# Kernel tuning notes

Hardware: AMD Instinct MI355X
Metric: run time of the kernel (lower is better)

Reference implementation:

```python
import jax, jax.numpy as jnp
import numpy as np

N, E = 50000, 800000
IN_C, HID, OUT_C = 128, 128, 64
EPS = 1e-5


def layer_norm(x, gamma, beta):
    mu = jnp.mean(x, axis=-1, keepdims=True)
    var = jnp.mean(jnp.square(x - mu), axis=-1, keepdims=True)
    return (x - mu) * jax.lax.rsqrt(var + EPS) * gamma + beta


def sage_conv(h, src, dst, W_l, b_l, W_r):
    # PyG SAGEConv (aggr='mean'): out = lin_l(mean_{j in N(i)} h_j) + lin_r(h_i)
    msg = h[src]                                                   # [E, HID] gather
    s = jax.ops.segment_sum(msg, dst, num_segments=N)              # [N, HID]
    cnt = jax.ops.segment_sum(jnp.ones((src.shape[0], 1), h.dtype), dst, num_segments=N)
    mean = s / jnp.maximum(cnt, 1.0)
    return mean @ W_l + b_l + h @ W_r


def setup_inputs() -> dict:
    key = jax.random.key(0)
    ks = jax.random.split(key, 12)
    sd_in = 1.0 / np.sqrt(IN_C)
    sd_h = 1.0 / np.sqrt(HID)
    return {
        "x": jax.random.normal(ks[0], (N, IN_C), jnp.float32),
        "edge_index": jax.random.randint(ks[1], (2, E), 0, N, jnp.int32),
        "edge_attr": jax.random.normal(ks[2], (E, IN_C), jnp.float32),
        "W_ne": jax.random.uniform(ks[3], (IN_C, HID), jnp.float32, -sd_in, sd_in),
        "b_ne": jax.random.uniform(ks[4], (HID,), jnp.float32, -sd_in, sd_in),
        "W_l": jax.random.uniform(ks[5], (HID, HID), jnp.float32, -sd_h, sd_h),
        "b_l": jax.random.uniform(ks[6], (HID,), jnp.float32, -sd_h, sd_h),
        "W_r": jax.random.uniform(ks[7], (HID, HID), jnp.float32, -sd_h, sd_h),
        "gamma": jnp.ones((HID,), jnp.float32),
        "beta": jnp.zeros((HID,), jnp.float32),
        "W_lin": jax.random.uniform(ks[8], (HID, OUT_C), jnp.float32, -sd_h, sd_h),
        "b_lin": jax.random.uniform(ks[9], (OUT_C,), jnp.float32, -sd_h, sd_h),
    }


def reference(x, edge_index, edge_attr, W_ne, b_ne, W_l, b_l, W_r, gamma, beta, W_lin, b_lin):
    src, dst = edge_index[0], edge_index[1]
    # node encoder
    h = x @ W_ne + b_ne
    # pre-conv with layers[0].conv
    h = sage_conv(h, src, dst, W_l, b_l, W_r)
    # layers[0] is unfixed: LN -> ReLU -> dropout(eval=id) -> conv -> residual
    r = layer_norm(h, gamma, beta)
    r = jax.nn.relu(r)
    h = sage_conv(r, src, dst, W_l, b_l, W_r) + h
    # layers[1:] are fixed -> identity
    # final norm/act/dropout(eval=id)/lin (reuses layers[0].norm/act)
    o = jax.nn.relu(layer_norm(h, gamma, beta))
    return o @ W_lin + b_lin
```

## Files before the change

### kernel.cpp

```cpp
#include <hip/hip_runtime.h>

typedef __attribute__((ext_vector_type(8))) short bf16x8;
typedef __attribute__((ext_vector_type(4))) float f32x4;

constexpr float LN_EPS = 1e-5f;

__device__ inline ushort f2bf(float f) {
  uint u = __float_as_uint(f);
  u += 0x7FFF + ((u >> 16) & 1);
  return (ushort)(u >> 16);
}
__device__ inline float bflo(uint u) { return __uint_as_float(u << 16); }
__device__ inline float bfhi(uint u) { return __uint_as_float(u & 0xFFFF0000u); }
__device__ inline uint pk2(float lo, float hi) { return (uint)f2bf(lo) | ((uint)f2bf(hi) << 16); }

struct Params {
  const float* x; const int* ei;
  const float *W_ne, *b_ne, *W_l, *b_l, *W_r, *gamma, *beta, *W_lin, *b_lin;
  float* out;
  ushort *Qbf, *H1, *Dbf, *xbf, *WAt, *WBt, *Wlt, *Wrt, *Wlint;
  signed char* Aq;
  float* Ascale;
  float *bA, *bB;
  int *cnt, *incl, *rowptr, *cursor, *bsums, *srclist;
  int N, E, nbS, nbT;
};


__global__ __launch_bounds__(256) void k_hist(Params p) {
  int e = blockIdx.x * 256 + threadIdx.x;
  if (e < p.E) atomicAdd(&p.cnt[p.ei[p.E + e]], 1);
}

__global__ __launch_bounds__(256) void k_p2(Params p) {
  __shared__ int sh[256];
  const int tid = threadIdx.x, bid = blockIdx.x;
  if (bid < p.nbS) {
    int i = bid * 256 + tid;
    int v = (i < p.N) ? p.cnt[i] : 0;
    sh[tid] = v;
    __syncthreads();
    for (int off = 1; off < 256; off <<= 1) {
      int t = (tid >= off) ? sh[tid - off] : 0;
      __syncthreads();
      sh[tid] += t;
      __syncthreads();
    }
    if (i < p.N) p.incl[i] = sh[tid];
    if (tid == 255) p.bsums[bid] = sh[255];
  } else if (bid < p.nbS + 129) {
    int blk = bid - p.nbS;
    float* srow = (float*)sh;
    const float* src = (blk < 128) ? (p.W_ne + blk * 128) : p.b_ne;
    if (tid < 128) srow[tid] = src[tid];
    __syncthreads();
    int col = tid & 127;
    const float* Wx = (tid < 128) ? p.W_l : p.W_r;
    float acc = 0.f;
#pragma unroll 8
    for (int k = 0; k < 128; ++k) acc = fmaf(srow[k], Wx[k * 128 + col], acc);
    if (blk < 128) {
      ushort* dst = (tid < 128) ? p.WAt : p.WBt;
      dst[col * 128 + blk] = f2bf(acc);
    } else {
      float* dst = (tid < 128) ? p.bA : p.bB;
      dst[col] = acc;
    }
  } else {
    const int nx16 = p.N * 16;
    const int total = nx16 + 16384 + 16384 + 8192;
    const int i0 = (bid - (p.nbS + 129)) * 256 + tid;
    const int st = (gridDim.x - (p.nbS + 129)) * 256;
    const float4* xin = (const float4*)p.x;
    uint4* xo = (uint4*)p.xbf;
    for (int idx = i0; idx < total; idx += st) {
      if (idx < nx16) {
        float4 a = xin[2 * (size_t)idx], b = xin[2 * (size_t)idx + 1];
        uint4 v;
        v.x = pk2(a.x, a.y); v.y = pk2(a.z, a.w);
        v.z = pk2(b.x, b.y); v.w = pk2(b.z, b.w);
        xo[idx] = v;
        continue;
      }
      int t = idx - nx16;
      if (t < 16384) { p.Wlt[(t & 127) * 128 + (t >> 7)] = f2bf(p.W_l[t]); continue; }
      t -= 16384;
      if (t < 16384) { p.Wrt[(t & 127) * 128 + (t >> 7)] = f2bf(p.W_r[t]); continue; }
      t -= 16384;
      p.Wlint[(t & 63) * 128 + (t >> 6)] = f2bf(p.W_lin[t]);
    }
  }
}

__global__ __launch_bounds__(256) void k_fill(Params p) {
  int e = blockIdx.x * 256 + threadIdx.x;
  if (e >= p.E) return;
  int s = p.ei[e], d = p.ei[p.E + e];
  int pos = atomicAdd(&p.cursor[d], 1);
  p.srclist[pos] = s;
}


template <int NCOL, int OMODE>
__device__ __forceinline__ void gemm_tile(const ushort* __restrict__ X, const ushort* __restrict__ Wt,
                                          const float* __restrict__ bias, void* __restrict__ Yv,
                                          float* __restrict__ Yscale, int M, int tile, char* ldsraw) {
  constexpr int NF = NCOL / 32;
  const int tid = threadIdx.x;
  const int wave = tid >> 6, lane = tid & 63;
  const int rbase = (wave >> 1) * 64;
  const int cbase = (wave & 1) * (NCOL / 2);
  const int lrow = lane & 15;
  const int lkb = (lane >> 4) * 8;
  const int row0 = tile * 128;

  size_t rIdx[4];
#pragma unroll
  for (int mf = 0; mf < 4; ++mf) {
    int r = row0 + rbase + mf * 16 + lrow;
    rIdx[mf] = (size_t)((r < M) ? r : (M - 1));
  }

  f32x4 acc[4][NF];
#pragma unroll
  for (int mf = 0; mf < 4; ++mf)
#pragma unroll
    for (int nf = 0; nf < NF; ++nf) acc[mf][nf] = (f32x4){0.f, 0.f, 0.f, 0.f};

#pragma unroll
  for (int ks = 0; ks < 4; ++ks) {
    bf16x8 a[4], b[NF];
#pragma unroll
    for (int mf = 0; mf < 4; ++mf)
      a[mf] = *(const bf16x8*)(X + rIdx[mf] * 128 + ks * 32 + lkb);
#pragma unroll
    for (int nf = 0; nf < NF; ++nf)
      b[nf] = *(const bf16x8*)(Wt + (size_t)(cbase + nf * 16 + lrow) * 128 + ks * 32 + lkb);
#pragma unroll
    for (int mf = 0; mf < 4; ++mf)
#pragma unroll
      for (int nf = 0; nf < NF; ++nf)
        acc[mf][nf] = __builtin_amdgcn_mfma_f32_16x16x32_bf16(a[mf], b[nf], acc[mf][nf], 0, 0, 0);
  }

  if (bias) {
#pragma unroll
    for (int nf = 0; nf < NF; ++nf) {
      float bv = bias[cbase + nf * 16 + lrow];
#pragma unroll
      for (int mf = 0; mf < 4; ++mf)
#pragma unroll
        for (int r = 0; r < 4; ++r) acc[mf][nf][r] += bv;
    }
  }

  if constexpr (OMODE == 2) {
    float (*rmaxh)[2] = (float(*)[2])ldsraw;
    signed char (*qt)[128] = (signed char(*)[128])(ldsraw + 1024);
#pragma unroll
    for (int mf = 0; mf < 4; ++mf)
#pragma unroll
      for (int r = 0; r < 4; ++r) {
        float m = 0.f;
#pragma unroll
        for (int nf = 0; nf < NF; ++nf) m = fmaxf(m, fabsf(acc[mf][nf][r]));
#pragma unroll
        for (int off = 1; off < 16; off <<= 1) m = fmaxf(m, __shfl_xor(m, off, 64));
        int lr = rbase + mf * 16 + (lane >> 4) * 4 + r;
        if (lrow == 0) rmaxh[lr][wave & 1] = m;
      }
    __syncthreads();
#pragma unroll
    for (int mf = 0; mf < 4; ++mf)
#pragma unroll
      for (int r = 0; r < 4; ++r) {
        int lr = rbase + mf * 16 + (lane >> 4) * 4 + r;
        float mx = fmaxf(rmaxh[lr][0], rmaxh[lr][1]);
        float inv = (mx > 0.f) ? 127.f / mx : 0.f;
#pragma unroll
        for (int nf = 0; nf < NF; ++nf)
          qt[lr][cbase + nf * 16 + lrow] = (signed char)__float2int_rn(acc[mf][nf][r] * inv);
      }
    __syncthreads();
    signed char* Yq = (signed char*)Yv;
    for (int idx = tid; idx < 1024; idx += 256) {
      int lr = idx >> 3, co = (idx & 7) * 16;
      int grow = row0 + lr;
      if (grow < M) *(uint4*)(Yq + (size_t)grow * 128 + co) = *(const uint4*)&qt[lr][co];
    }
    if (tid < 128) {
      int grow = row0 + tid;
      if (grow < M) Yscale[grow] = fmaxf(rmaxh[tid][0], rmaxh[tid][1]) * (1.f / 127.f);
    }
    return;
  }

#pragma unroll
  for (int nf = 0; nf < NF; ++nf) {
    int col = cbase + nf * 16 + lrow;
#pragma unroll
    for (int mf = 0; mf < 4; ++mf) {
      int growb = row0 + rbase + mf * 16 + (lane >> 4) * 4;
#pragma unroll
      for (int r = 0; r < 4; ++r) {
        int grow = growb + r;
        if (grow < M) {
          float val = acc[mf][nf][r];
          if constexpr (OMODE == 1)
            ((ushort*)Yv)[(size_t)grow * NCOL + col] = f2bf(val);
          else
            ((float*)Yv)[(size_t)grow * NCOL + col] = val;
        }
      }
    }
  }
}

__global__ __launch_bounds__(256) void k_p4(Params p) {
  __shared__ __align__(16) char qlds[1024 + 16384];
  const int bid = blockIdx.x, tid = threadIdx.x;
  if (bid < p.nbS) {
    int* ss = (int*)qlds;
    int v = (tid < bid) ? p.bsums[tid] : 0;
    ss[tid] = v;
    __syncthreads();
    for (int off = 128; off > 0; off >>= 1) {
      if (tid < off) ss[tid] += ss[tid + off];
      __syncthreads();
    }
    int prefix = ss[0];
    int i = bid * 256 + tid;
    if (i < p.N) {
      int inc = p.incl[i] + prefix;
      p.rowptr[i + 1] = inc;
      p.cursor[i] = inc - p.cnt[i];
    }
    if (i == 0) p.rowptr[0] = 0;
    return;
  }
  int job = bid - p.nbS;
  if (job < p.nbT) gemm_tile<128, 2>(p.xbf, p.WAt, p.bA, p.Aq, p.Ascale, p.N, job, qlds);
  else gemm_tile<128, 1>(p.xbf, p.WBt, p.bB, p.Qbf, nullptr, p.N, job - p.nbT, qlds);
}

__global__ __launch_bounds__(256) void k_gemm2(Params p) {
  __shared__ __align__(16) char qlds[1024 + 16384];
  int job = blockIdx.y * p.nbT + blockIdx.x;
  if (job < p.nbT) gemm_tile<128, 2>(p.Dbf, p.Wlt, nullptr, p.Aq, p.Ascale, p.N, job, qlds);
  else gemm_tile<128, 1>(p.Dbf, p.Wrt, nullptr, p.Qbf, nullptr, p.N, job - p.nbT, qlds);
}

__global__ __launch_bounds__(256) void k_gout(Params p) {
  gemm_tile<64, 0>(p.Dbf, p.Wlint, p.b_lin, p.out, nullptr, p.N, blockIdx.x, nullptr);
}


__device__ __forceinline__ void acc8q(uint2 u, float sc, float* a) {
  a[0] = fmaf((float)(int)(signed char)(u.x & 0xFF), sc, a[0]);
  a[1] = fmaf((float)(int)(signed char)((u.x >> 8) & 0xFF), sc, a[1]);
  a[2] = fmaf((float)(int)(signed char)((u.x >> 16) & 0xFF), sc, a[2]);
  a[3] = fmaf((float)(int)(signed char)(u.x >> 24), sc, a[3]);
  a[4] = fmaf((float)(int)(signed char)(u.y & 0xFF), sc, a[4]);
  a[5] = fmaf((float)(int)(signed char)((u.y >> 8) & 0xFF), sc, a[5]);
  a[6] = fmaf((float)(int)(signed char)((u.y >> 16) & 0xFF), sc, a[6]);
  a[7] = fmaf((float)(int)(signed char)(u.y >> 24), sc, a[7]);
}

__device__ __forceinline__ void gather_mean(const signed char* __restrict__ Pq, const float* __restrict__ Psc,
                                            const int* __restrict__ rowptr, const int* __restrict__ srclist,
                                            int w, int lane, float* a) {
  int fl = lane & 15, g4 = lane >> 4;
  int beg = rowptr[w], end = rowptr[w + 1];
  for (int base = beg; base < end; base += 64) {
    int m = end - base;
    if (m > 64) m = 64;
    int sidx = (lane < m) ? srclist[base + lane] : 0;
    for (int i = 0; i < m; i += 16) {
      int j0 = i + g4, j1 = j0 + 4, j2 = j0 + 8, j3 = j0 + 12;
      int s0 = __shfl(sidx, j0 & 63, 64);
      int s1 = __shfl(sidx, j1 & 63, 64);
      int s2 = __shfl(sidx, j2 & 63, 64);
      int s3 = __shfl(sidx, j3 & 63, 64);
      float c0 = Psc[s0], c1 = Psc[s1], c2 = Psc[s2], c3 = Psc[s3];
      uint2 u0 = *(const uint2*)(Pq + (size_t)s0 * 128 + fl * 8);
      uint2 u1 = *(const uint2*)(Pq + (size_t)s1 * 128 + fl * 8);
      uint2 u2 = *(const uint2*)(Pq + (size_t)s2 * 128 + fl * 8);
      uint2 u3 = *(const uint2*)(Pq + (size_t)s3 * 128 + fl * 8);
      if (j0 < m) acc8q(u0, c0, a);
      if (j1 < m) acc8q(u1, c1, a);
      if (j2 < m) acc8q(u2, c2, a);
      if (j3 < m) acc8q(u3, c3, a);
    }
  }
#pragma unroll
  for (int k = 0; k < 8; ++k) {
    a[k] += __shfl_xor(a[k], 16, 64);
    a[k] += __shfl_xor(a[k], 32, 64);
  }
  float inv = 1.f / fmaxf((float)(end - beg), 1.f);
#pragma unroll
  for (int k = 0; k < 8; ++k) a[k] *= inv;
}

__device__ __forceinline__ void ln_relu8(const float* h, const float* __restrict__ gamma,
                                         const float* __restrict__ beta, int fl, float* o) {
  float sum = 0.f;
#pragma unroll
  for (int k = 0; k < 8; ++k) sum += h[k];
#pragma unroll
  for (int off = 1; off < 16; off <<= 1) sum += __shfl_xor(sum, off, 64);
  float mu = sum * (1.f / 128.f);
  float s2 = 0.f;
#pragma unroll
  for (int k = 0; k < 8; ++k) { float d = h[k] - mu; s2 += d * d; }
#pragma unroll
  for (int off = 1; off < 16; off <<= 1) s2 += __shfl_xor(s2, off, 64);
  float scale = rsqrtf(s2 * (1.f / 128.f) + LN_EPS);
  float4 g0 = *(const float4*)(gamma + fl * 8);
  float4 g1 = *(const float4*)(gamma + fl * 8 + 4);
  float4 b0 = *(const float4*)(beta + fl * 8);
  float4 b1 = *(const float4*)(beta + fl * 8 + 4);
  float gg[8] = {g0.x, g0.y, g0.z, g0.w, g1.x, g1.y, g1.z, g1.w};
  float bb[8] = {b0.x, b0.y, b0.z, b0.w, b1.x, b1.y, b1.z, b1.w};
#pragma unroll
  for (int k = 0; k < 8; ++k) o[k] = fmaxf((h[k] - mu) * scale * gg[k] + bb[k], 0.f);
}

__device__ __forceinline__ uint4 pack8(const float* v) {
  uint4 u;
  u.x = pk2(v[0], v[1]); u.y = pk2(v[2], v[3]);
  u.z = pk2(v[4], v[5]); u.w = pk2(v[6], v[7]);
  return u;
}

__global__ __launch_bounds__(256) void k_agg1(Params p) {
  int w = (blockIdx.x * 256 + threadIdx.x) >> 6;
  int lane = threadIdx.x & 63;
  if (w >= p.N) return;
  int fl = lane & 15;
  float a[8] = {0.f, 0.f, 0.f, 0.f, 0.f, 0.f, 0.f, 0.f};
  gather_mean(p.Aq, p.Ascale, p.rowptr, p.srclist, w, lane, a);
  uint4 qv = ((const uint4*)p.Qbf)[(size_t)w * 16 + fl];
  float4 bl0 = *(const float4*)(p.b_l + fl * 8);
  float4 bl1 = *(const float4*)(p.b_l + fl * 8 + 4);
  float q[8] = {bflo(qv.x), bfhi(qv.x), bflo(qv.y), bfhi(qv.y), bflo(qv.z), bfhi(qv.z), bflo(qv.w), bfhi(qv.w)};
  float bl[8] = {bl0.x, bl0.y, bl0.z, bl0.w, bl1.x, bl1.y, bl1.z, bl1.w};
  float h[8];
#pragma unroll
  for (int k = 0; k < 8; ++k) h[k] = a[k] + q[k] + bl[k];
  float r[8];
  ln_relu8(h, p.gamma, p.beta, fl, r);
  if (lane < 16) {
    ((uint4*)p.H1)[(size_t)w * 16 + fl] = pack8(h);
    ((uint4*)p.Dbf)[(size_t)w * 16 + fl] = pack8(r);
  }
}

__global__ __launch_bounds__(256) void k_agg2(Params p) {
  int w = (blockIdx.x * 256 + threadIdx.x) >> 6;
  int lane = threadIdx.x & 63;
  if (w >= p.N) return;
  int fl = lane & 15;
  float a[8] = {0.f, 0.f, 0.f, 0.f, 0.f, 0.f, 0.f, 0.f};
  gather_mean(p.Aq, p.Ascale, p.rowptr, p.srclist, w, lane, a);
  uint4 vv = ((const uint4*)p.Qbf)[(size_t)w * 16 + fl];
  uint4 hv = ((const uint4*)p.H1)[(size_t)w * 16 + fl];
  float4 bl0 = *(const float4*)(p.b_l + fl * 8);
  float4 bl1 = *(const float4*)(p.b_l + fl * 8 + 4);
  float vf[8] = {bflo(vv.x), bfhi(vv.x), bflo(vv.y), bfhi(vv.y), bflo(vv.z), bfhi(vv.z), bflo(vv.w), bfhi(vv.w)};
  float hf[8] = {bflo(hv.x), bfhi(hv.x), bflo(hv.y), bfhi(hv.y), bflo(hv.z), bfhi(hv.z), bflo(hv.w), bfhi(hv.w)};
  float bl[8] = {bl0.x, bl0.y, bl0.z, bl0.w, bl1.x, bl1.y, bl1.z, bl1.w};
  float h[8];
#pragma unroll
  for (int k = 0; k < 8; ++k) h[k] = a[k] + vf[k] + bl[k] + hf[k];
  float o[8];
  ln_relu8(h, p.gamma, p.beta, fl, o);
  if (lane < 16) ((uint4*)p.Dbf)[(size_t)w * 16 + fl] = pack8(o);
}


extern "C" void kernel_launch(void* const* d_in, const int* in_sizes, int n_in,
                              void* d_out, int out_size, void* d_ws, size_t ws_size,
                              hipStream_t stream) {
  Params p;
  p.x = (const float*)d_in[0];
  p.ei = (const int*)d_in[1];
  p.W_ne = (const float*)d_in[3];
  p.b_ne = (const float*)d_in[4];
  p.W_l = (const float*)d_in[5];
  p.b_l = (const float*)d_in[6];
  p.W_r = (const float*)d_in[7];
  p.gamma = (const float*)d_in[8];
  p.beta = (const float*)d_in[9];
  p.W_lin = (const float*)d_in[10];
  p.b_lin = (const float*)d_in[11];
  p.out = (float*)d_out;

  p.N = in_sizes[0] / 128;
  p.E = in_sizes[1] / 2;
  p.nbS = (p.N + 255) / 256;
  p.nbT = (p.N + 127) / 128;

  char* w = (char*)d_ws;
  const size_t S2 = (size_t)p.N * 128 * sizeof(ushort);
  p.Qbf = (ushort*)w;    w += S2;
  p.H1 = (ushort*)w;     w += S2;
  p.Dbf = (ushort*)w;    w += S2;
  p.xbf = (ushort*)w;    w += S2;
  p.Aq = (signed char*)w;  w += (size_t)p.N * 128;
  p.Ascale = (float*)w;  w += (size_t)p.N * sizeof(float);
  p.WAt = (ushort*)w;    w += 128 * 128 * sizeof(ushort);
  p.WBt = (ushort*)w;    w += 128 * 128 * sizeof(ushort);
  p.Wlt = (ushort*)w;    w += 128 * 128 * sizeof(ushort);
  p.Wrt = (ushort*)w;    w += 128 * 128 * sizeof(ushort);
  p.Wlint = (ushort*)w;  w += 64 * 128 * sizeof(ushort);
  p.bA = (float*)w;      w += 128 * sizeof(float);
  p.bB = (float*)w;      w += 128 * sizeof(float);
  p.cnt = (int*)w;       w += (size_t)p.N * sizeof(int);
  p.incl = (int*)w;      w += (size_t)p.N * sizeof(int);
  p.rowptr = (int*)w;    w += ((size_t)p.N + 4) * sizeof(int);
  p.cursor = (int*)w;    w += (size_t)p.N * sizeof(int);
  p.bsums = (int*)w;     w += 1024 * sizeof(int);
  p.srclist = (int*)w;

  const int nbE = (p.E + 255) / 256;
  const int nbW = ((p.N * 64) + 255) / 256;

  hipMemsetAsync(p.cnt, 0, (size_t)p.N * sizeof(int), stream);
  k_hist<<<nbE, 256, 0, stream>>>(p);
  k_p2<<<p.nbS + 129 + 1024, 256, 0, stream>>>(p);
  k_p4<<<p.nbS + 2 * p.nbT, 256, 0, stream>>>(p);
  k_fill<<<nbE, 256, 0, stream>>>(p);
  k_agg1<<<nbW, 256, 0, stream>>>(p);
  k_gemm2<<<dim3(p.nbT, 2), 256, 0, stream>>>(p);
  k_agg2<<<nbW, 256, 0, stream>>>(p);
  k_gout<<<p.nbT, 256, 0, stream>>>(p);
}
```

Before: 224.8 us.

## Fuse fp32-to-bf16 input conversion into GEMM and pair both weight GEMMs per tile

Removes the separate pass that converted x to a bf16 buffer, loading fp32 x directly in the first GEMM and packing to bf16 in registers. Each 64-row tile now computes both the lin_l (quantized int8) and lin_r (bf16) outputs in one block, with waves split by weight matrix instead of column halves. This reads the activation tile once for both products and drops one LDS barrier from the quantization path. In exchange, tiles are smaller, so weight fragments are reloaded more often relative to the rows processed.

```diff
diff --git a/kernel.cpp b/kernel.cpp
--- a/kernel.cpp
+++ b/kernel.cpp
@@ -18,12 +18,12 @@
   const float* x; const int* ei;
   const float *W_ne, *b_ne, *W_l, *b_l, *W_r, *gamma, *beta, *W_lin, *b_lin;
   float* out;
-  ushort *Qbf, *H1, *Dbf, *xbf, *WAt, *WBt, *Wlt, *Wrt, *Wlint;
+  ushort *Qbf, *H1, *Dbf, *WAt, *WBt, *Wlt, *Wrt, *Wlint;
   signed char* Aq;
   float* Ascale;
   float *bA, *bB;
   int *cnt, *incl, *rowptr, *cursor, *bsums, *srclist;
-  int N, E, nbS, nbT;
+  int N, E, nbS, nbT, nbT2;
 };
 
 
@@ -67,22 +67,11 @@
       dst[col] = acc;
     }
   } else {
-    const int nx16 = p.N * 16;
-    const int total = nx16 + 16384 + 16384 + 8192;
+    const int total = 16384 + 16384 + 8192;
     const int i0 = (bid - (p.nbS + 129)) * 256 + tid;
     const int st = (gridDim.x - (p.nbS + 129)) * 256;
-    const float4* xin = (const float4*)p.x;
-    uint4* xo = (uint4*)p.xbf;
     for (int idx = i0; idx < total; idx += st) {
-      if (idx < nx16) {
-        float4 a = xin[2 * (size_t)idx], b = xin[2 * (size_t)idx + 1];
-        uint4 v;
-        v.x = pk2(a.x, a.y); v.y = pk2(a.z, a.w);
-        v.z = pk2(b.x, b.y); v.w = pk2(b.z, b.w);
-        xo[idx] = v;
-        continue;
-      }
-      int t = idx - nx16;
+      int t = idx;
       if (t < 16384) { p.Wlt[(t & 127) * 128 + (t >> 7)] = f2bf(p.W_l[t]); continue; }
       t -= 16384;
       if (t < 16384) { p.Wrt[(t & 127) * 128 + (t >> 7)] = f2bf(p.W_r[t]); continue; }
@@ -101,126 +90,120 @@
 }
 
 
-template <int NCOL, int OMODE>
-__device__ __forceinline__ void gemm_tile(const ushort* __restrict__ X, const ushort* __restrict__ Wt,
-                                          const float* __restrict__ bias, void* __restrict__ Yv,
-                                          float* __restrict__ Yscale, int M, int tile, char* ldsraw) {
-  constexpr int NF = NCOL / 32;
+template <bool F32A>
+__device__ __forceinline__ void gemm_pair_tile(const void* __restrict__ Xv,
+                                               const ushort* __restrict__ Wt1, const ushort* __restrict__ Wt2,
+                                               const float* __restrict__ bias1, const float* __restrict__ bias2,
+                                               signed char* __restrict__ Yq, float* __restrict__ Yscale,
+                                               ushort* __restrict__ Ybf, int M, int tile,
+                                               signed char (*qt)[128]) {
   const int tid = threadIdx.x;
   const int wave = tid >> 6, lane = tid & 63;
-  const int rbase = (wave >> 1) * 64;
-  const int cbase = (wave & 1) * (NCOL / 2);
+  const int rbase = (wave >> 1) * 32;
+  const int chalf = wave & 1;
+  const ushort* Wt = chalf ? Wt2 : Wt1;
+  const float* bias = chalf ? bias2 : bias1;
   const int lrow = lane & 15;
   const int lkb = (lane >> 4) * 8;
-  const int row0 = tile * 128;
-
-  size_t rIdx[4];
-#pragma unroll
-  for (int mf = 0; mf < 4; ++mf) {
+  const int row0 = tile * 64;
+
+  size_t rIdx[2];
+#pragma unroll
+  for (int mf = 0; mf < 2; ++mf) {
     int r = row0 + rbase + mf * 16 + lrow;
     rIdx[mf] = (size_t)((r < M) ? r : (M - 1));
   }
 
-  f32x4 acc[4][NF];
-#pragma unroll
-  for (int mf = 0; mf < 4; ++mf)
-#pragma unroll
-    for (int nf = 0; nf < NF; ++nf) acc[mf][nf] = (f32x4){0.f, 0.f, 0.f, 0.f};
+  f32x4 acc[2][8];
+#pragma unroll
+  for (int mf = 0; mf < 2; ++mf)
+#pragma unroll
+    for (int nf = 0; nf < 8; ++nf) acc[mf][nf] = (f32x4){0.f, 0.f, 0.f, 0.f};
 
 #pragma unroll
   for (int ks = 0; ks < 4; ++ks) {
-    bf16x8 a[4], b[NF];
-#pragma unroll
-    for (int mf = 0; mf < 4; ++mf)
-      a[mf] = *(const bf16x8*)(X + rIdx[mf] * 128 + ks * 32 + lkb);
-#pragma unroll
-    for (int nf = 0; nf < NF; ++nf)
-      b[nf] = *(const bf16x8*)(Wt + (size_t)(cbase + nf * 16 + lrow) * 128 + ks * 32 + lkb);
-#pragma unroll
-    for (int mf = 0; mf < 4; ++mf)
-#pragma unroll
-      for (int nf = 0; nf < NF; ++nf)
+    bf16x8 a[2], b[8];
+#pragma unroll
+    for (int mf = 0; mf < 2; ++mf) {
+      if constexpr (F32A) {
+        const float* Xf = (const float*)Xv + rIdx[mf] * 128 + ks * 32 + lkb;
+        float4 lo = *(const float4*)Xf;
+        float4 hi = *(const float4*)(Xf + 4);
+        uint4 v;
+        v.x = pk2(lo.x, lo.y); v.y = pk2(lo.z, lo.w);
+        v.z = pk2(hi.x, hi.y); v.w = pk2(hi.z, hi.w);
+        a[mf] = *reinterpret_cast<bf16x8*>(&v);
+      } else {
+        a[mf] = *(const bf16x8*)((const ushort*)Xv + rIdx[mf] * 128 + ks * 32 + lkb);
+      }
+    }
+#pragma unroll
+    for (int nf = 0; nf < 8; ++nf)
+      b[nf] = *(const bf16x8*)(Wt + (size_t)(nf * 16 + lrow) * 128 + ks * 32 + lkb);
+#pragma unroll
+    for (int mf = 0; mf < 2; ++mf)
+#pragma unroll
+      for (int nf = 0; nf < 8; ++nf)
         acc[mf][nf] = __builtin_amdgcn_mfma_f32_16x16x32_bf16(a[mf], b[nf], acc[mf][nf], 0, 0, 0);
   }
 
   if (bias) {
 #pragma unroll
-    for (int nf = 0; nf < NF; ++nf) {
-      float bv = bias[cbase + nf * 16 + lrow];
-#pragma unroll
-      for (int mf = 0; mf < 4; ++mf)
+    for (int nf = 0; nf < 8; ++nf) {
+      float bv = bias[nf * 16 + lrow];
+#pragma unroll
+      for (int mf = 0; mf < 2; ++mf)
 #pragma unroll
         for (int r = 0; r < 4; ++r) acc[mf][nf][r] += bv;
     }
   }
 
-  if constexpr (OMODE == 2) {
-    float (*rmaxh)[2] = (float(*)[2])ldsraw;
-    signed char (*qt)[128] = (signed char(*)[128])(ldsraw + 1024);
-#pragma unroll
-    for (int mf = 0; mf < 4; ++mf)
+  if (chalf == 0) {
+#pragma unroll
+    for (int mf = 0; mf < 2; ++mf)
 #pragma unroll
       for (int r = 0; r < 4; ++r) {
         float m = 0.f;
 #pragma unroll
-        for (int nf = 0; nf < NF; ++nf) m = fmaxf(m, fabsf(acc[mf][nf][r]));
+        for (int nf = 0; nf < 8; ++nf) m = fmaxf(m, fabsf(acc[mf][nf][r]));
 #pragma unroll
         for (int off = 1; off < 16; off <<= 1) m = fmaxf(m, __shfl_xor(m, off, 64));
         int lr = rbase + mf * 16 + (lane >> 4) * 4 + r;
-        if (lrow == 0) rmaxh[lr][wave & 1] = m;
+        float inv = (m > 0.f) ? 127.f / m : 0.f;
+#pragma unroll
+        for (int nf = 0; nf < 8; ++nf)
+          qt[lr][nf * 16 + lrow] = (signed char)__float2int_rn(acc[mf][nf][r] * inv);
+        int grow = row0 + lr;
+        if (lrow == 0 && grow < M) Yscale[grow] = m * (1.f / 127.f);
       }
-    __syncthreads();
-#pragma unroll
-    for (int mf = 0; mf < 4; ++mf)
-#pragma unroll
-      for (int r = 0; r < 4; ++r) {
-        int lr = rbase + mf * 16 + (lane >> 4) * 4 + r;
-        float mx = fmaxf(rmaxh[lr][0], rmaxh[lr][1]);
-        float inv = (mx > 0.f) ? 127.f / mx : 0.f;
-#pragma unroll
-        for (int nf = 0; nf < NF; ++nf)
-          qt[lr][cbase + nf * 16 + lrow] = (signed char)__float2int_rn(acc[mf][nf][r] * inv);
-      }
-    __syncthreads();
-    signed char* Yq = (signed char*)Yv;
-    for (int idx = tid; idx < 1024; idx += 256) {
-      int lr = idx >> 3, co = (idx & 7) * 16;
-      int grow = row0 + lr;
-      if (grow < M) *(uint4*)(Yq + (size_t)grow * 128 + co) = *(const uint4*)&qt[lr][co];
-    }
-    if (tid < 128) {
-      int grow = row0 + tid;
-      if (grow < M) Yscale[grow] = fmaxf(rmaxh[tid][0], rmaxh[tid][1]) * (1.f / 127.f);
-    }
-    return;
-  }
-
-#pragma unroll
-  for (int nf = 0; nf < NF; ++nf) {
-    int col = cbase + nf * 16 + lrow;
-#pragma unroll
-    for (int mf = 0; mf < 4; ++mf) {
-      int growb = row0 + rbase + mf * 16 + (lane >> 4) * 4;
-#pragma unroll
-      for (int r = 0; r < 4; ++r) {
-        int grow = growb + r;
-        if (grow < M) {
-          float val = acc[mf][nf][r];
-          if constexpr (OMODE == 1)
-            ((ushort*)Yv)[(size_t)grow * NCOL + col] = f2bf(val);
-          else
-            ((float*)Yv)[(size_t)grow * NCOL + col] = val;
+  } else {
+#pragma unroll
+    for (int nf = 0; nf < 8; ++nf) {
+      int col = nf * 16 + lrow;
+#pragma unroll
+      for (int mf = 0; mf < 2; ++mf) {
+        int growb = row0 + rbase + mf * 16 + (lane >> 4) * 4;
+#pragma unroll
+        for (int r = 0; r < 4; ++r) {
+          int grow = growb + r;
+          if (grow < M) Ybf[(size_t)grow * 128 + col] = f2bf(acc[mf][nf][r]);
         }
       }
     }
   }
+  __syncthreads();
+  for (int idx = tid; idx < 512; idx += 256) {
+    int lr = idx >> 3, co = (idx & 7) * 16;
+    int grow = row0 + lr;
+    if (grow < M) *(uint4*)(Yq + (size_t)grow * 128 + co) = *(const uint4*)&qt[lr][co];
+  }
 }
 
 __global__ __launch_bounds__(256) void k_p4(Params p) {
-  __shared__ __align__(16) char qlds[1024 + 16384];
+  __shared__ __align__(16) signed char qt[64][128];
   const int bid = blockIdx.x, tid = threadIdx.x;
   if (bid < p.nbS) {
-    int* ss = (int*)qlds;
+    int* ss = (int*)qt;
     int v = (tid < bid) ? p.bsums[tid] : 0;
     ss[tid] = v;
     __syncthreads();
@@ -238,20 +221,65 @@
     if (i == 0) p.rowptr[0] = 0;
     return;
   }
-  int job = bid - p.nbS;
-  if (job < p.nbT) gemm_tile<128, 2>(p.xbf, p.WAt, p.bA, p.Aq, p.Ascale, p.N, job, qlds);
-  else gemm_tile<128, 1>(p.xbf, p.WBt, p.bB, p.Qbf, nullptr, p.N, job - p.nbT, qlds);
+  gemm_pair_tile<true>(p.x, p.WAt, p.WBt, p.bA, p.bB, p.Aq, p.Ascale, p.Qbf, p.N, bid - p.nbS, qt);
 }
 
 __global__ __launch_bounds__(256) void k_gemm2(Params p) {
-  __shared__ __align__(16) char qlds[1024 + 16384];
-  int job = blockIdx.y * p.nbT + blockIdx.x;
-  if (job < p.nbT) gemm_tile<128, 2>(p.Dbf, p.Wlt, nullptr, p.Aq, p.Ascale, p.N, job, qlds);
-  else gemm_tile<128, 1>(p.Dbf, p.Wrt, nullptr, p.Qbf, nullptr, p.N, job - p.nbT, qlds);
-}
+  __shared__ __align__(16) signed char qt[64][128];
+  gemm_pair_tile<false>(p.Dbf, p.Wlt, p.Wrt, nullptr, nullptr, p.Aq, p.Ascale, p.Qbf, p.N, blockIdx.x, qt);
+}
+
 
 __global__ __launch_bounds__(256) void k_gout(Params p) {
-  gemm_tile<64, 0>(p.Dbf, p.Wlint, p.b_lin, p.out, nullptr, p.N, blockIdx.x, nullptr);
+  const int tid = threadIdx.x;
+  const int wave = tid >> 6, lane = tid & 63;
+  const int rbase = (wave >> 1) * 64;
+  const int cbase = (wave & 1) * 32;
+  const int lrow = lane & 15;
+  const int lkb = (lane >> 4) * 8;
+  const int row0 = blockIdx.x * 128;
+  const ushort* X = p.Dbf;
+
+  size_t rIdx[4];
+#pragma unroll
+  for (int mf = 0; mf < 4; ++mf) {
+    int r = row0 + rbase + mf * 16 + lrow;
+    rIdx[mf] = (size_t)((r < p.N) ? r : (p.N - 1));
+  }
+  f32x4 acc[4][2];
+#pragma unroll
+  for (int mf = 0; mf < 4; ++mf)
+#pragma unroll
+    for (int nf = 0; nf < 2; ++nf) acc[mf][nf] = (f32x4){0.f, 0.f, 0.f, 0.f};
+#pragma unroll
+  for (int ks = 0; ks < 4; ++ks) {
+    bf16x8 a[4], b[2];
+#pragma unroll
+    for (int mf = 0; mf < 4; ++mf)
+      a[mf] = *(const bf16x8*)(X + rIdx[mf] * 128 + ks * 32 + lkb);
+#pragma unroll
+    for (int nf = 0; nf < 2; ++nf)
+      b[nf] = *(const bf16x8*)(p.Wlint + (size_t)(cbase + nf * 16 + lrow) * 128 + ks * 32 + lkb);
+#pragma unroll
+    for (int mf = 0; mf < 4; ++mf)
+#pragma unroll
+      for (int nf = 0; nf < 2; ++nf)
+        acc[mf][nf] = __builtin_amdgcn_mfma_f32_16x16x32_bf16(a[mf], b[nf], acc[mf][nf], 0, 0, 0);
+  }
+#pragma unroll
+  for (int nf = 0; nf < 2; ++nf) {
+    int col = cbase + nf * 16 + lrow;
+    float bv = p.b_lin[col];
+#pragma unroll
+    for (int mf = 0; mf < 4; ++mf) {
+      int growb = row0 + rbase + mf * 16 + (lane >> 4) * 4;
+#pragma unroll
+      for (int r = 0; r < 4; ++r) {
+        int grow = growb + r;
+        if (grow < p.N) p.out[(size_t)grow * 64 + col] = acc[mf][nf][r] + bv;
+      }
+    }
+  }
 }
 
 
@@ -400,13 +428,13 @@
   p.E = in_sizes[1] / 2;
   p.nbS = (p.N + 255) / 256;
   p.nbT = (p.N + 127) / 128;
+  p.nbT2 = (p.N + 63) / 64;
 
   char* w = (char*)d_ws;
   const size_t S2 = (size_t)p.N * 128 * sizeof(ushort);
   p.Qbf = (ushort*)w;    w += S2;
   p.H1 = (ushort*)w;     w += S2;
   p.Dbf = (ushort*)w;    w += S2;
-  p.xbf = (ushort*)w;    w += S2;
   p.Aq = (signed char*)w;  w += (size_t)p.N * 128;
   p.Ascale = (float*)w;  w += (size_t)p.N * sizeof(float);
   p.WAt = (ushort*)w;    w += 128 * 128 * sizeof(ushort);
@@ -428,11 +456,11 @@
 
   hipMemsetAsync(p.cnt, 0, (size_t)p.N * sizeof(int), stream);
   k_hist<<<nbE, 256, 0, stream>>>(p);
-  k_p2<<<p.nbS + 129 + 1024, 256, 0, stream>>>(p);
-  k_p4<<<p.nbS + 2 * p.nbT, 256, 0, stream>>>(p);
+  k_p2<<<p.nbS + 129 + 64, 256, 0, stream>>>(p);
+  k_p4<<<p.nbS + p.nbT2, 256, 0, stream>>>(p);
   k_fill<<<nbE, 256, 0, stream>>>(p);
   k_agg1<<<nbW, 256, 0, stream>>>(p);
-  k_gemm2<<<dim3(p.nbT, 2), 256, 0, stream>>>(p);
+  k_gemm2<<<p.nbT2, 256, 0, stream>>>(p);
   k_agg2<<<nbW, 256, 0, stream>>>(p);
   k_gout<<<p.nbT, 256, 0, stream>>>(p);
 }
```

New measurement: 234.5 us. +4.3%, slower.

## Reschedule CSR build phases to overlap histogram with weight prep and scan with GEMM

Applied to the files above, without the earlier changes.

Moves the edge histogram into the same launch as weight folding and x conversion, and moves the per-block scan into the launch with the first GEMM tiles. The cross-block prefix fixup becomes its own small kernel before the fill step. The aim is to hide the short atomic and scan phases behind independent work, at the same number of launches. The dependency order is still correct because each scan step runs in a later launch than the step it reads from.

```diff
diff --git a/kernel.cpp b/kernel.cpp
--- a/kernel.cpp
+++ b/kernel.cpp
@@ -23,34 +23,18 @@
   float* Ascale;
   float *bA, *bB;
   int *cnt, *incl, *rowptr, *cursor, *bsums, *srclist;
-  int N, E, nbS, nbT;
+  int N, E, nbS, nbT, nbE;
 };
 
 
-__global__ __launch_bounds__(256) void k_hist(Params p) {
-  int e = blockIdx.x * 256 + threadIdx.x;
-  if (e < p.E) atomicAdd(&p.cnt[p.ei[p.E + e]], 1);
-}
-
-__global__ __launch_bounds__(256) void k_p2(Params p) {
-  __shared__ int sh[256];
+__global__ __launch_bounds__(256) void k_m1(Params p) {
+  __shared__ float srow[128];
   const int tid = threadIdx.x, bid = blockIdx.x;
-  if (bid < p.nbS) {
-    int i = bid * 256 + tid;
-    int v = (i < p.N) ? p.cnt[i] : 0;
-    sh[tid] = v;
-    __syncthreads();
-    for (int off = 1; off < 256; off <<= 1) {
-      int t = (tid >= off) ? sh[tid - off] : 0;
-      __syncthreads();
-      sh[tid] += t;
-      __syncthreads();
-    }
-    if (i < p.N) p.incl[i] = sh[tid];
-    if (tid == 255) p.bsums[bid] = sh[255];
-  } else if (bid < p.nbS + 129) {
-    int blk = bid - p.nbS;
-    float* srow = (float*)sh;
+  if (bid < p.nbE) {
+    int e = bid * 256 + tid;
+    if (e < p.E) atomicAdd(&p.cnt[p.ei[p.E + e]], 1);
+  } else if (bid < p.nbE + 129) {
+    int blk = bid - p.nbE;
     const float* src = (blk < 128) ? (p.W_ne + blk * 128) : p.b_ne;
     if (tid < 128) srow[tid] = src[tid];
     __syncthreads();
@@ -69,8 +53,8 @@
   } else {
     const int nx16 = p.N * 16;
     const int total = nx16 + 16384 + 16384 + 8192;
-    const int i0 = (bid - (p.nbS + 129)) * 256 + tid;
-    const int st = (gridDim.x - (p.nbS + 129)) * 256;
+    const int i0 = (bid - (p.nbE + 129)) * 256 + tid;
+    const int st = (gridDim.x - (p.nbE + 129)) * 256;
     const float4* xin = (const float4*)p.x;
     uint4* xo = (uint4*)p.xbf;
     for (int idx = i0; idx < total; idx += st) {
@@ -92,14 +76,6 @@
   }
 }
 
-__global__ __launch_bounds__(256) void k_fill(Params p) {
-  int e = blockIdx.x * 256 + threadIdx.x;
-  if (e >= p.E) return;
-  int s = p.ei[e], d = p.ei[p.E + e];
-  int pos = atomicAdd(&p.cursor[d], 1);
-  p.srclist[pos] = s;
-}
-
 
 template <int NCOL, int OMODE>
 __device__ __forceinline__ void gemm_tile(const ushort* __restrict__ X, const ushort* __restrict__ Wt,
@@ -216,31 +192,58 @@
   }
 }
 
-__global__ __launch_bounds__(256) void k_p4(Params p) {
+
+__global__ __launch_bounds__(256) void k_m2(Params p) {
   __shared__ __align__(16) char qlds[1024 + 16384];
   const int bid = blockIdx.x, tid = threadIdx.x;
   if (bid < p.nbS) {
-    int* ss = (int*)qlds;
-    int v = (tid < bid) ? p.bsums[tid] : 0;
-    ss[tid] = v;
+    int* sh = (int*)qlds;
+    int i = bid * 256 + tid;
+    int v = (i < p.N) ? p.cnt[i] : 0;
+    sh[tid] = v;
     __syncthreads();
-    for (int off = 128; off > 0; off >>= 1) {
-      if (tid < off) ss[tid] += ss[tid + off];
+    for (int off = 1; off < 256; off <<= 1) {
+      int t = (tid >= off) ? sh[tid - off] : 0;
       __syncthreads();
-    }
-    int prefix = ss[0];
-    int i = bid * 256 + tid;
-    if (i < p.N) {
-      int inc = p.incl[i] + prefix;
-      p.rowptr[i + 1] = inc;
-      p.cursor[i] = inc - p.cnt[i];
-    }
-    if (i == 0) p.rowptr[0] = 0;
+      sh[tid] += t;
+      __syncthreads();
+    }
+    if (i < p.N) p.incl[i] = sh[tid];
+    if (tid == 255) p.bsums[bid] = sh[255];
     return;
   }
   int job = bid - p.nbS;
   if (job < p.nbT) gemm_tile<128, 2>(p.xbf, p.WAt, p.bA, p.Aq, p.Ascale, p.N, job, qlds);
   else gemm_tile<128, 1>(p.xbf, p.WBt, p.bB, p.Qbf, nullptr, p.N, job - p.nbT, qlds);
+}
+
+
+__global__ __launch_bounds__(256) void k_m3(Params p) {
+  __shared__ int ss[256];
+  const int bid = blockIdx.x, tid = threadIdx.x;
+  int v = (tid < bid) ? p.bsums[tid] : 0;
+  ss[tid] = v;
+  __syncthreads();
+  for (int off = 128; off > 0; off >>= 1) {
+    if (tid < off) ss[tid] += ss[tid + off];
+    __syncthreads();
+  }
+  int prefix = ss[0];
+  int i = bid * 256 + tid;
+  if (i < p.N) {
+    int inc = p.incl[i] + prefix;
+    p.rowptr[i + 1] = inc;
+    p.cursor[i] = inc - p.cnt[i];
+  }
+  if (i == 0) p.rowptr[0] = 0;
+}
+
+__global__ __launch_bounds__(256) void k_fill(Params p) {
+  int e = blockIdx.x * 256 + threadIdx.x;
+  if (e >= p.E) return;
+  int s = p.ei[e], d = p.ei[p.E + e];
+  int pos = atomicAdd(&p.cursor[d], 1);
+  p.srclist[pos] = s;
 }
 
 __global__ __launch_bounds__(256) void k_gemm2(Params p) {
@@ -400,6 +403,7 @@
   p.E = in_sizes[1] / 2;
   p.nbS = (p.N + 255) / 256;
   p.nbT = (p.N + 127) / 128;
+  p.nbE = (p.E + 255) / 256;
 
   char* w = (char*)d_ws;
   const size_t S2 = (size_t)p.N * 128 * sizeof(ushort);
@@ -423,14 +427,13 @@
   p.bsums = (int*)w;     w += 1024 * sizeof(int);
   p.srclist = (int*)w;
 
-  const int nbE = (p.E + 255) / 256;
   const int nbW = ((p.N * 64) + 255) / 256;
 
   hipMemsetAsync(p.cnt, 0, (size_t)p.N * sizeof(int), stream);
-  k_hist<<<nbE, 256, 0, stream>>>(p);
-  k_p2<<<p.nbS + 129 + 1024, 256, 0, stream>>>(p);
-  k_p4<<<p.nbS + 2 * p.nbT, 256, 0, stream>>>(p);
-  k_fill<<<nbE, 256, 0, stream>>>(p);
+  k_m1<<<p.nbE + 129 + 1024, 256, 0, stream>>>(p);
+  k_m2<<<p.nbS + 2 * p.nbT, 256, 0, stream>>>(p);
+  k_m3<<<p.nbS, 256, 0, stream>>>(p);
+  k_fill<<<p.nbE, 256, 0, stream>>>(p);
   k_agg1<<<nbW, 256, 0, stream>>>(p);
   k_gemm2<<<dim3(p.nbT, 2), 256, 0, stream>>>(p);
   k_agg2<<<nbW, 256, 0, stream>>>(p);
```

Result: faster. 219.1 us, median of 2 (-2.5%).
